# Kernel optimization log

Hardware: AMD Instinct MI355X
Metric: run time of the kernel (lower is better)

Reference implementation:

```python
import jax, jax.numpy as jnp
import numpy as np

IN, OUT, RANK = 512, 1024, 8
STEPS = 8  # fixed-step RK4 integration of the geodesic ODE over t in [0, 1]


def setup_inputs() -> dict:
    key = jax.random.key(0)
    ks = jax.random.split(key, 8)
    scale = 0.05
    x = jax.random.normal(ks[0], (8, 4096, IN), jnp.float32)
    # orthogonal init of U_0 [OUT, IN] (orthonormal columns, tall matrix)
    U0 = jnp.linalg.qr(jax.random.normal(ks[1], (OUT, IN), jnp.float32))[0]
    Wa = scale * jax.random.normal(ks[2], (IN, RANK), jnp.float32)
    La = scale * jax.random.normal(ks[3], (IN, RANK), jnp.float32)
    Ra = scale * jax.random.normal(ks[4], (IN, RANK), jnp.float32)
    Wb = scale * jax.random.normal(ks[5], (IN, RANK), jnp.float32)
    Lb = scale * jax.random.normal(ks[6], (OUT - IN, RANK), jnp.float32)
    Rb = scale * jax.random.normal(ks[7], (IN, RANK), jnp.float32)
    return {"x": x, "U0": U0, "Wa": Wa, "La": La, "Ra": Ra,
            "Wb": Wb, "Lb": Lb, "Rb": Rb}


def _geodesic_solve(U0, A, G):
    # Integrate dU/dt = U @ A + G, U(0) = U0, with RK4 over unit time.
    dt = 1.0 / STEPS
    f = lambda U: U @ A + G
    def step(U, _):
        k1 = f(U)
        k2 = f(U + 0.5 * dt * k1)
        k3 = f(U + 0.5 * dt * k2)
        k4 = f(U + dt * k3)
        return U + (dt / 6.0) * (k1 + 2.0 * k2 + 2.0 * k3 + k4), None
    U, _ = jax.lax.scan(step, U0, None, length=STEPS)
    return U


def reference(x, U0, Wa, La, Ra, Wb, Lb, Rb):
    # z: pooled context [B, IN]
    z = x.mean(axis=1)
    # low-rank controller -> skew-symmetric Lie-algebra drift A [IN, IN]
    a = z @ Wa                                      # [B, R]
    A = jnp.einsum('br,ir,jr->bij', a, La, Ra)      # [B, IN, IN]
    A_avg = (A - jnp.swapaxes(A, 1, 2)).mean(axis=0)  # skew, batch-averaged
    # low-rank forcing B [B, OUT-IN, IN], batch-averaged
    b = z @ Wb                                      # [B, R]
    B_avg = jnp.einsum('br,or,jr->boj', b, Lb, Rb).mean(axis=0)
    # pad top with zeros -> G [OUT, IN]
    G = jnp.concatenate([jnp.zeros((IN, IN), x.dtype), B_avg], axis=0)
    # geodesic/Lie ODE solve for the dynamic weight W [OUT, IN]
    W = _geodesic_solve(U0, A_avg, G)
    # final dense projection
    return x @ W.T
```

## Files before the change

kernel.cpp:

```cpp
#include <hip/hip_runtime.h>
#include <hip/hip_bf16.h>
#include <type_traits>
#include <cstdint>

#define IN_DIM   512
#define OUT_DIM  1024
#define RANKP    8
#define MROWS    32768

typedef float f32x4 __attribute__((ext_vector_type(4)));
typedef short s8vec __attribute__((ext_vector_type(8)));
typedef __bf16 b8vec __attribute__((ext_vector_type(8)));

template <typename V, typename = void>
struct mfma_ok : std::false_type {};
template <typename V>
struct mfma_ok<V, std::void_t<decltype(__builtin_amdgcn_mfma_f32_16x16x32_bf16(
    std::declval<V>(), std::declval<V>(), std::declval<f32x4>(), 0, 0, 0))>>
    : std::true_type {};
using frag_t = std::conditional_t<mfma_ok<s8vec>::value, s8vec, b8vec>;

__device__ __forceinline__ void async_copy16(void* lds, const void* g) {
    __builtin_amdgcn_global_load_lds(
        (const __attribute__((address_space(1))) void*)(uintptr_t)g,
        (__attribute__((address_space(3))) void*)(uint32_t)(uintptr_t)lds,
        16, 0, 0);
}

__device__ __forceinline__ unsigned short f2bf(float f) {
    unsigned int u = __float_as_uint(f);
    unsigned int r = (u + 0x7fffu + ((u >> 16) & 1u)) >> 16;
    return (unsigned short)r;
}

__global__ void __launch_bounds__(256) geo_k1(const float* __restrict__ x,
                                              unsigned short* __restrict__ xh,
                                              const float* __restrict__ Wa,
                                              const float* __restrict__ Wb,
                                              float* __restrict__ gsum) {
    const int tid  = threadIdx.x;
    const int c4   = (tid & 127) * 4;
    const int half = tid >> 7;
    const int r0   = blockIdx.x * 32 + half * 16;
    float4 s = {0.f, 0.f, 0.f, 0.f};
    for (int i = 0; i < 16; ++i) {
        const size_t base = (size_t)(r0 + i) * IN_DIM + c4;
        float4 v = *(const float4*)(x + base);
        s.x += v.x; s.y += v.y; s.z += v.z; s.w += v.w;
        ushort4 h;
        h.x = f2bf(v.x); h.y = f2bf(v.y); h.z = f2bf(v.z); h.w = f2bf(v.w);
        *(ushort4*)(xh + base) = h;
    }
    const float* wa = Wa + (size_t)c4 * 8;
    const float* wb = Wb + (size_t)c4 * 8;
    float av[8], bv[8];
#pragma unroll
    for (int r = 0; r < 8; ++r) {
        av[r] = s.x * wa[r] + s.y * wa[8 + r] + s.z * wa[16 + r] + s.w * wa[24 + r];
        bv[r] = s.x * wb[r] + s.y * wb[8 + r] + s.z * wb[16 + r] + s.w * wb[24 + r];
    }
#pragma unroll
    for (int off = 32; off; off >>= 1) {
#pragma unroll
        for (int r = 0; r < 8; ++r) {
            av[r] += __shfl_xor(av[r], off, 64);
            bv[r] += __shfl_xor(bv[r], off, 64);
        }
    }
    __shared__ float wred[4][16];
    const int lane = tid & 63, wave = tid >> 6;
    if (lane == 0) {
#pragma unroll
        for (int r = 0; r < 8; ++r) { wred[wave][r] = av[r]; wred[wave][8 + r] = bv[r]; }
    }
    __syncthreads();
    if (tid < 16) {
        float t = wred[0][tid] + wred[1][tid] + wred[2][tid] + wred[3][tid];
        atomicAdd(&gsum[tid], t);
    }
}

__global__ void geo_k2a(const float* __restrict__ gsum, const float* __restrict__ La,
                        const float* __restrict__ Ra, const float* __restrict__ Lb,
                        float* __restrict__ Vws, float* __restrict__ Lbp) {
    const int tid = threadIdx.x;
    const int i = blockIdx.x * 32 + (tid >> 3);
    const int r = tid & 7;
    const float sc = 1.0f / 32768.0f;
    const float ar = gsum[r] * sc;
    const float br = gsum[8 + r] * sc;
    Vws[i * 16 + r]     = ar * La[i * 8 + r];
    Vws[i * 16 + 8 + r] = Ra[i * 8 + r];
    Lbp[i * 8 + r]      = br * Lb[i * 8 + r];
}

__global__ void geo_k2b(const float* __restrict__ Vws, const float* __restrict__ Rb,
                        float* __restrict__ Gg, float* __restrict__ Zg) {
    __shared__ float sX[16][24];
    const int tid = threadIdx.x;
    const int i0 = blockIdx.x * 16;
    for (int e = tid; e < 384; e += 256) {
        const int row = e / 24, col = e - row * 24;
        sX[row][col] = (col < 16) ? Vws[(i0 + row) * 16 + col]
                                  : Rb[(i0 + row) * 8 + col - 16];
    }
    __syncthreads();
    {
        const int u = tid >> 4, v = tid & 15;
        float s = 0.f;
#pragma unroll
        for (int k = 0; k < 16; ++k) s += sX[k][u] * sX[k][v];
        atomicAdd(&Gg[tid], s);
    }
    if (tid < 128) {
        const int r = tid >> 4, u = tid & 15;
        float s = 0.f;
#pragma unroll
        for (int k = 0; k < 16; ++k) s += sX[k][16 + r] * sX[k][u];
        atomicAdd(&Zg[tid], s);
    }
}

__device__ __forceinline__ void mm16(float (*D)[16], float (*A)[16], float (*B)[16]) {
    const int tid = threadIdx.x;
    const int i = tid >> 4, j = tid & 15;
    float s = 0.f;
#pragma unroll
    for (int k = 0; k < 16; ++k) s += A[i][k] * B[k][j];
    __syncthreads();
    D[i][j] = s;
    __syncthreads();
}

__global__ void geo_k2c(const float* __restrict__ Gg, const float* __restrict__ Zg,
                        const float* __restrict__ Vws, const float* __restrict__ Rb,
                        float* __restrict__ VPws, float* __restrict__ RRws) {
    __shared__ float G16[16][16], Jm[16][16];
    __shared__ float C2m[16][16], C3m[16][16], C4m[16][16];
    __shared__ float Cp[16][16], Cq[16][16];
    __shared__ float Pi[16][16], Xi[16][16], T1[16][16], T2[16][16], Ct[16][16];
    __shared__ float Zm[8][16], Em[8][16];
    const int tid = threadIdx.x;
    const int i = tid >> 4, j = tid & 15;

    G16[i][j] = Gg[tid];
    float jm = 0.f;
    if (i < 8 && j == i + 8) jm = 1.f;
    if (i >= 8 && j == i - 8) jm = -1.f;
    Jm[i][j] = jm;
    if (tid < 128) Zm[tid >> 4][tid & 15] = Zg[tid];
    __syncthreads();

    mm16(T1, Jm, G16);  mm16(C2m, T1, Jm);
    mm16(T1, C2m, G16); mm16(C3m, T1, Jm);
    mm16(T1, C3m, G16); mm16(C4m, T1, Jm);

    const float h  = 0.125f;
    const float c1 = h, c2 = h * h * 0.5f, c3 = h * h * h * (1.f / 6.f),
                c4 = h * h * h * h * (1.f / 24.f);
    Cp[i][j] = c1 * Jm[i][j] + c2 * C2m[i][j] + c3 * C3m[i][j] + c4 * C4m[i][j];
    Cq[i][j] = c2 * Jm[i][j] + c3 * C2m[i][j] + c4 * C3m[i][j];
    Xi[i][j] = 0.f;
    __syncthreads();
    Pi[i][j] = Cp[i][j];
    __syncthreads();

    for (int it = 0; it < 7; ++it) {
        mm16(T1, Pi, G16);
        mm16(T2, T1, Cp);
        const float pij = Pi[i][j];
        Xi[i][j] += pij;
        Pi[i][j] = pij + Cp[i][j] + T2[i][j];
        __syncthreads();
    }

    mm16(T1, Cq, G16);
    mm16(T2, T1, Xi);
    Ct[i][j] = 8.f * Cq[i][j] + h * Xi[i][j] + T2[i][j];
    __syncthreads();

    if (tid < 128) {
        const int r = tid >> 4, u = tid & 15;
        float s = 0.f;
#pragma unroll
        for (int t = 0; t < 16; ++t) s += Zm[r][t] * Ct[t][u];
        Em[r][u] = s;
    }
    __syncthreads();

#pragma unroll
    for (int rr = 0; rr < 2; ++rr) {
        const int row = tid * 2 + rr;
        const float* vr = Vws + row * 16;
        float v[16];
#pragma unroll
        for (int q = 0; q < 4; ++q) {
            float4 t4 = *(const float4*)(vr + q * 4);
            v[q * 4] = t4.x; v[q * 4 + 1] = t4.y; v[q * 4 + 2] = t4.z; v[q * 4 + 3] = t4.w;
        }
#pragma unroll
        for (int u = 0; u < 16; ++u) {
            float s = 0.f;
#pragma unroll
            for (int k = 0; k < 16; ++k) s += v[k] * Pi[k][u];
            VPws[row * 16 + u] = s;
        }
#pragma unroll
        for (int r = 0; r < 8; ++r) {
            float s = Rb[row * 8 + r];
#pragma unroll
            for (int u = 0; u < 16; ++u) s += Em[r][u] * v[u];
            RRws[r * IN_DIM + row] = s;
        }
    }
}

__global__ void __launch_bounds__(256) geo_k34(const float* __restrict__ U0,
                                               const float* __restrict__ Vws,
                                               const float* __restrict__ VPws,
                                               const float* __restrict__ Lbp,
                                               const float* __restrict__ RRws,
                                               unsigned short* __restrict__ wh) {
    const int o   = blockIdx.x;
    const int tid = threadIdx.x;
    const int j0  = tid * 2;
    const float2 u0 = *(const float2*)(U0 + (size_t)o * IN_DIM + j0);

    const float* vpa = VPws + j0 * 16;
    const float* vpb = vpa + 16;
    float p[16];
#pragma unroll
    for (int u = 0; u < 16; ++u) p[u] = u0.x * vpa[u] + u0.y * vpb[u];
#pragma unroll
    for (int off = 32; off; off >>= 1) {
#pragma unroll
        for (int u = 0; u < 16; ++u) p[u] += __shfl_xor(p[u], off, 64);
    }
    __shared__ float wred[4][16];
    __shared__ float sY[16];
    const int lane = tid & 63, wave = tid >> 6;
    if (lane == 0) {
#pragma unroll
        for (int u = 0; u < 16; ++u) wred[wave][u] = p[u];
    }
    __syncthreads();
    if (tid < 16) sY[tid] = wred[0][tid] + wred[1][tid] + wred[2][tid] + wred[3][tid];
    __syncthreads();

    const float* va = Vws + j0 * 16;
    const float* vb = va + 16;
    float w0 = u0.x, w1 = u0.y;
#pragma unroll
    for (int u = 0; u < 16; ++u) {
        const float s = sY[u];
        w0 += s * va[u];
        w1 += s * vb[u];
    }
    if (o >= IN_DIM) {
        const int op = o - IN_DIM;
#pragma unroll
        for (int r = 0; r < 8; ++r) {
            const float lb = Lbp[op * 8 + r];
            w0 += lb * RRws[r * IN_DIM + j0];
            w1 += lb * RRws[r * IN_DIM + j0 + 1];
        }
    }
    ushort2 hv;
    hv.x = f2bf(w0); hv.y = f2bf(w1);
    *(ushort2*)(wh + (size_t)o * IN_DIM + j0) = hv;
}

__global__ void __launch_bounds__(256) geo_k5_gemm(const __hip_bfloat16* __restrict__ A,
                                                   const __hip_bfloat16* __restrict__ B,
                                                   float* __restrict__ C) {
    __shared__ __hip_bfloat16 As[128 * 32];
    __shared__ __hip_bfloat16 Bs[128 * 32];
    const int tid  = threadIdx.x;
    const int m0   = blockIdx.x * 128;
    const int n0   = blockIdx.y * 128;
    const int lane = tid & 63;
    const int wave = tid >> 6;
    const int wm   = (wave >> 1) * 64;
    const int wn   = (wave & 1) * 64;

    const int srow = tid >> 2;
    const int scol = (tid & 3) * 8;
    const __hip_bfloat16* gA0 = A + (size_t)(m0 + srow) * IN_DIM + scol;
    const __hip_bfloat16* gA1 = A + (size_t)(m0 + 64 + srow) * IN_DIM + scol;
    const __hip_bfloat16* gB0 = B + (size_t)(n0 + srow) * IN_DIM + scol;
    const __hip_bfloat16* gB1 = B + (size_t)(n0 + 64 + srow) * IN_DIM + scol;
    __hip_bfloat16* lA0 = As + (size_t)tid * 8;
    __hip_bfloat16* lA1 = As + (size_t)(tid + 256) * 8;
    __hip_bfloat16* lB0 = Bs + (size_t)tid * 8;
    __hip_bfloat16* lB1 = Bs + (size_t)(tid + 256) * 8;

    f32x4 acc[4][4];
#pragma unroll
    for (int t = 0; t < 4; ++t)
#pragma unroll
        for (int s = 0; s < 4; ++s) acc[t][s] = (f32x4){0.f, 0.f, 0.f, 0.f};

    const int aoff = (wm + (lane & 15)) * 32 + (lane >> 4) * 8;
    const int boff = (wn + (lane & 15)) * 32 + (lane >> 4) * 8;

    for (int kt = 0; kt < 16; ++kt) {
        const int k0 = kt * 32;
        __syncthreads();
        async_copy16(lA0, gA0 + k0);
        async_copy16(lA1, gA1 + k0);
        async_copy16(lB0, gB0 + k0);
        async_copy16(lB1, gB1 + k0);
        __syncthreads();

        frag_t af[4], bfr[4];
#pragma unroll
        for (int t = 0; t < 4; ++t) af[t] = *(const frag_t*)(As + aoff + t * 16 * 32);
#pragma unroll
        for (int s = 0; s < 4; ++s) bfr[s] = *(const frag_t*)(Bs + boff + s * 16 * 32);
#pragma unroll
        for (int t = 0; t < 4; ++t)
#pragma unroll
            for (int s = 0; s < 4; ++s)
                acc[t][s] = __builtin_amdgcn_mfma_f32_16x16x32_bf16(af[t], bfr[s], acc[t][s], 0, 0, 0);
    }

    const int cm = m0 + wm + (lane >> 4) * 4;
    const int cn = n0 + wn + (lane & 15);
#pragma unroll
    for (int t = 0; t < 4; ++t)
#pragma unroll
        for (int s = 0; s < 4; ++s)
#pragma unroll
            for (int v = 0; v < 4; ++v)
                C[(size_t)(cm + t * 16 + v) * OUT_DIM + cn + s * 16] = acc[t][s][v];
}

extern "C" void kernel_launch(void* const* d_in, const int* in_sizes, int n_in,
                              void* d_out, int out_size, void* d_ws, size_t ws_size,
                              hipStream_t stream) {
    const float* x  = (const float*)d_in[0];
    const float* U0 = (const float*)d_in[1];
    const float* Wa = (const float*)d_in[2];
    const float* La = (const float*)d_in[3];
    const float* Ra = (const float*)d_in[4];
    const float* Wb = (const float*)d_in[5];
    const float* Lb = (const float*)d_in[6];
    const float* Rb = (const float*)d_in[7];
    float* out = (float*)d_out;

    char* ws = (char*)d_ws;
    unsigned short* xh  = (unsigned short*)(ws);
    unsigned short* wh  = (unsigned short*)(ws + 33554432);
    float* acc  = (float*)(ws + 34603008);
    float* gsum = acc;
    float* Gg   = acc + 16;
    float* Zg   = acc + 272;
    float* Vws  = (float*)(ws + 34605056);
    float* Lbp  = (float*)(ws + 34637824);
    float* RRws = (float*)(ws + 34654208);
    float* VPws = (float*)(ws + 34670592);

    hipMemsetAsync(acc, 0, 2048, stream);
    geo_k1<<<1024, 256, 0, stream>>>(x, xh, Wa, Wb, gsum);
    geo_k2a<<<16, 256, 0, stream>>>(gsum, La, Ra, Lb, Vws, Lbp);
    geo_k2b<<<32, 256, 0, stream>>>(Vws, Rb, Gg, Zg);
    geo_k2c<<<1, 256, 0, stream>>>(Gg, Zg, Vws, Rb, VPws, RRws);
    geo_k34<<<1024, 256, 0, stream>>>(U0, Vws, VPws, Lbp, RRws, wh);
    geo_k5_gemm<<<dim3(256, 8), 256, 0, stream>>>((const __hip_bfloat16*)xh,
                                                  (const __hip_bfloat16*)wh, out);
}
```

Baseline: 312.0 us.

## Fuse small setup kernels into one block and widen GEMM K-tile with LDS swizzle

Replaces the memset plus atomic reductions and three small kernels (k2a, k2b, k2c) with per-block partial sums from k1 and a single one-block kernel that reduces them, builds V, computes the Gram matrices and the closed-form propagators. The goal is to cut launch overhead and atomic traffic. The GEMM separately doubles its K tile to 64 with an XOR-swizzled LDS layout, halving the number of barrier/load rounds and avoiding bank conflicts. The single-block kernel now does a serial 512-long Gram reduction, which adds some latency on one CU.

```diff
diff --git a/kernel.cpp b/kernel.cpp
--- a/kernel.cpp
+++ b/kernel.cpp
@@ -5,7 +5,6 @@
 
 #define IN_DIM   512
 #define OUT_DIM  1024
-#define RANKP    8
 #define MROWS    32768
 
 typedef float f32x4 __attribute__((ext_vector_type(4)));
@@ -37,7 +36,7 @@
                                               unsigned short* __restrict__ xh,
                                               const float* __restrict__ Wa,
                                               const float* __restrict__ Wb,
-                                              float* __restrict__ gsum) {
+                                              float* __restrict__ part) {
     const int tid  = threadIdx.x;
     const int c4   = (tid & 127) * 4;
     const int half = tid >> 7;
@@ -74,51 +73,9 @@
         for (int r = 0; r < 8; ++r) { wred[wave][r] = av[r]; wred[wave][8 + r] = bv[r]; }
     }
     __syncthreads();
-    if (tid < 16) {
-        float t = wred[0][tid] + wred[1][tid] + wred[2][tid] + wred[3][tid];
-        atomicAdd(&gsum[tid], t);
-    }
-}
-
-__global__ void geo_k2a(const float* __restrict__ gsum, const float* __restrict__ La,
-                        const float* __restrict__ Ra, const float* __restrict__ Lb,
-                        float* __restrict__ Vws, float* __restrict__ Lbp) {
-    const int tid = threadIdx.x;
-    const int i = blockIdx.x * 32 + (tid >> 3);
-    const int r = tid & 7;
-    const float sc = 1.0f / 32768.0f;
-    const float ar = gsum[r] * sc;
-    const float br = gsum[8 + r] * sc;
-    Vws[i * 16 + r]     = ar * La[i * 8 + r];
-    Vws[i * 16 + 8 + r] = Ra[i * 8 + r];
-    Lbp[i * 8 + r]      = br * Lb[i * 8 + r];
-}
-
-__global__ void geo_k2b(const float* __restrict__ Vws, const float* __restrict__ Rb,
-                        float* __restrict__ Gg, float* __restrict__ Zg) {
-    __shared__ float sX[16][24];
-    const int tid = threadIdx.x;
-    const int i0 = blockIdx.x * 16;
-    for (int e = tid; e < 384; e += 256) {
-        const int row = e / 24, col = e - row * 24;
-        sX[row][col] = (col < 16) ? Vws[(i0 + row) * 16 + col]
-                                  : Rb[(i0 + row) * 8 + col - 16];
-    }
-    __syncthreads();
-    {
-        const int u = tid >> 4, v = tid & 15;
-        float s = 0.f;
-#pragma unroll
-        for (int k = 0; k < 16; ++k) s += sX[k][u] * sX[k][v];
-        atomicAdd(&Gg[tid], s);
-    }
-    if (tid < 128) {
-        const int r = tid >> 4, u = tid & 15;
-        float s = 0.f;
-#pragma unroll
-        for (int k = 0; k < 16; ++k) s += sX[k][16 + r] * sX[k][u];
-        atomicAdd(&Zg[tid], s);
-    }
+    if (tid < 16)
+        part[(size_t)blockIdx.x * 16 + tid] =
+            wred[0][tid] + wred[1][tid] + wred[2][tid] + wred[3][tid];
 }
 
 __device__ __forceinline__ void mm16(float (*D)[16], float (*A)[16], float (*B)[16]) {
@@ -132,9 +89,19 @@
     __syncthreads();
 }
 
-__global__ void geo_k2c(const float* __restrict__ Gg, const float* __restrict__ Zg,
-                        const float* __restrict__ Vws, const float* __restrict__ Rb,
-                        float* __restrict__ VPws, float* __restrict__ RRws) {
+__global__ void __launch_bounds__(256) geo_k2(const float* __restrict__ part,
+                                              const float* __restrict__ La,
+                                              const float* __restrict__ Ra,
+                                              const float* __restrict__ Lb,
+                                              const float* __restrict__ Rb,
+                                              float* __restrict__ Vws,
+                                              float* __restrict__ Lbp,
+                                              float* __restrict__ VPws,
+                                              float* __restrict__ RRws) {
+    __shared__ float sV[IN_DIM][16];
+    __shared__ float sRb[IN_DIM][8];
+    __shared__ float red2[16][16];
+    __shared__ float gs[16];
     __shared__ float G16[16][16], Jm[16][16];
     __shared__ float C2m[16][16], C3m[16][16], C4m[16][16];
     __shared__ float Cp[16][16], Cq[16][16];
@@ -143,12 +110,52 @@
     const int tid = threadIdx.x;
     const int i = tid >> 4, j = tid & 15;
 
-    G16[i][j] = Gg[tid];
-    float jm = 0.f;
-    if (i < 8 && j == i + 8) jm = 1.f;
-    if (i >= 8 && j == i - 8) jm = -1.f;
-    Jm[i][j] = jm;
-    if (tid < 128) Zm[tid >> 4][tid & 15] = Zg[tid];
+    {
+        const int u = tid & 15, c = tid >> 4;
+        float s = 0.f;
+        for (int q = 0; q < 64; ++q) s += part[(size_t)(c * 64 + q) * 16 + u];
+        red2[c][u] = s;
+    }
+    __syncthreads();
+    if (tid < 16) {
+        float s = 0.f;
+#pragma unroll
+        for (int c = 0; c < 16; ++c) s += red2[c][tid];
+        gs[tid] = s * (1.0f / 32768.0f);
+    }
+    __syncthreads();
+
+    for (int rr = 0; rr < 2; ++rr) {
+        const int row = tid * 2 + rr;
+#pragma unroll
+        for (int r = 0; r < 8; ++r) {
+            const float vl = gs[r] * La[row * 8 + r];
+            const float vr = Ra[row * 8 + r];
+            sV[row][r]     = vl;
+            sV[row][8 + r] = vr;
+            Vws[row * 16 + r]     = vl;
+            Vws[row * 16 + 8 + r] = vr;
+            sRb[row][r] = Rb[row * 8 + r];
+            Lbp[row * 8 + r] = gs[8 + r] * Lb[row * 8 + r];
+        }
+    }
+    __syncthreads();
+
+    {
+        float s = 0.f;
+        for (int k = 0; k < IN_DIM; ++k) s += sV[k][i] * sV[k][j];
+        G16[i][j] = s;
+        float jm = 0.f;
+        if (i < 8 && j == i + 8) jm = 1.f;
+        if (i >= 8 && j == i - 8) jm = -1.f;
+        Jm[i][j] = jm;
+    }
+    if (tid < 128) {
+        const int r = tid >> 4, u = tid & 15;
+        float s = 0.f;
+        for (int k = 0; k < IN_DIM; ++k) s += sRb[k][r] * sV[k][u];
+        Zm[r][u] = s;
+    }
     __syncthreads();
 
     mm16(T1, Jm, G16);  mm16(C2m, T1, Jm);
@@ -191,13 +198,9 @@
 #pragma unroll
     for (int rr = 0; rr < 2; ++rr) {
         const int row = tid * 2 + rr;
-        const float* vr = Vws + row * 16;
         float v[16];
 #pragma unroll
-        for (int q = 0; q < 4; ++q) {
-            float4 t4 = *(const float4*)(vr + q * 4);
-            v[q * 4] = t4.x; v[q * 4 + 1] = t4.y; v[q * 4 + 2] = t4.z; v[q * 4 + 3] = t4.w;
-        }
+        for (int k = 0; k < 16; ++k) v[k] = sV[row][k];
 #pragma unroll
         for (int u = 0; u < 16; ++u) {
             float s = 0.f;
@@ -207,7 +210,7 @@
         }
 #pragma unroll
         for (int r = 0; r < 8; ++r) {
-            float s = Rb[row * 8 + r];
+            float s = sRb[row][r];
 #pragma unroll
             for (int u = 0; u < 16; ++u) s += Em[r][u] * v[u];
             RRws[r * IN_DIM + row] = s;
@@ -273,8 +276,8 @@
 __global__ void __launch_bounds__(256) geo_k5_gemm(const __hip_bfloat16* __restrict__ A,
                                                    const __hip_bfloat16* __restrict__ B,
                                                    float* __restrict__ C) {
-    __shared__ __hip_bfloat16 As[128 * 32];
-    __shared__ __hip_bfloat16 Bs[128 * 32];
+    __shared__ __hip_bfloat16 As[128 * 64];
+    __shared__ __hip_bfloat16 Bs[128 * 64];
     const int tid  = threadIdx.x;
     const int m0   = blockIdx.x * 128;
     const int n0   = blockIdx.y * 128;
@@ -283,16 +286,21 @@
     const int wm   = (wave >> 1) * 64;
     const int wn   = (wave & 1) * 64;
 
-    const int srow = tid >> 2;
-    const int scol = (tid & 3) * 8;
-    const __hip_bfloat16* gA0 = A + (size_t)(m0 + srow) * IN_DIM + scol;
-    const __hip_bfloat16* gA1 = A + (size_t)(m0 + 64 + srow) * IN_DIM + scol;
-    const __hip_bfloat16* gB0 = B + (size_t)(n0 + srow) * IN_DIM + scol;
-    const __hip_bfloat16* gB1 = B + (size_t)(n0 + 64 + srow) * IN_DIM + scol;
-    __hip_bfloat16* lA0 = As + (size_t)tid * 8;
-    __hip_bfloat16* lA1 = As + (size_t)(tid + 256) * 8;
-    __hip_bfloat16* lB0 = Bs + (size_t)tid * 8;
-    __hip_bfloat16* lB1 = Bs + (size_t)(tid + 256) * 8;
+    const int rowoff = lane >> 3;
+    const int gcol   = ((lane & 7) ^ rowoff) * 8;
+    const __hip_bfloat16* gA[4];
+    const __hip_bfloat16* gB[4];
+    char* lA[4];
+    char* lB[4];
+#pragma unroll
+    for (int j2 = 0; j2 < 4; ++j2) {
+        const int ri  = wave * 4 + j2;
+        const int row = ri * 8 + rowoff;
+        gA[j2] = A + (size_t)(m0 + row) * IN_DIM + gcol;
+        gB[j2] = B + (size_t)(n0 + row) * IN_DIM + gcol;
+        lA[j2] = (char*)As + ri * 1024 + lane * 16;
+        lB[j2] = (char*)Bs + ri * 1024 + lane * 16;
+    }
 
     f32x4 acc[4][4];
 #pragma unroll
@@ -300,28 +308,37 @@
 #pragma unroll
         for (int s = 0; s < 4; ++s) acc[t][s] = (f32x4){0.f, 0.f, 0.f, 0.f};
 
-    const int aoff = (wm + (lane & 15)) * 32 + (lane >> 4) * 8;
-    const int boff = (wn + (lane & 15)) * 32 + (lane >> 4) * 8;
-
-    for (int kt = 0; kt < 16; ++kt) {
-        const int k0 = kt * 32;
+    const int frow = lane & 15;
+    const int fsw  = lane & 7;
+    const int fk   = lane >> 4;
+
+    for (int kt = 0; kt < 8; ++kt) {
+        const int k0 = kt * 64;
         __syncthreads();
-        async_copy16(lA0, gA0 + k0);
-        async_copy16(lA1, gA1 + k0);
-        async_copy16(lB0, gB0 + k0);
-        async_copy16(lB1, gB1 + k0);
+#pragma unroll
+        for (int j2 = 0; j2 < 4; ++j2) {
+            async_copy16(lA[j2], gA[j2] + k0);
+            async_copy16(lB[j2], gB[j2] + k0);
+        }
         __syncthreads();
 
-        frag_t af[4], bfr[4];
-#pragma unroll
-        for (int t = 0; t < 4; ++t) af[t] = *(const frag_t*)(As + aoff + t * 16 * 32);
-#pragma unroll
-        for (int s = 0; s < 4; ++s) bfr[s] = *(const frag_t*)(Bs + boff + s * 16 * 32);
-#pragma unroll
-        for (int t = 0; t < 4; ++t)
+#pragma unroll
+        for (int h = 0; h < 2; ++h) {
+            frag_t af[4], bfr[4];
+#pragma unroll
+            for (int t = 0; t < 4; ++t)
+                af[t] = *(const frag_t*)((const char*)As +
+                        (size_t)(wm + t * 16 + frow) * 128 + (((h * 4 + fk) ^ fsw) * 16));
 #pragma unroll
             for (int s = 0; s < 4; ++s)
-                acc[t][s] = __builtin_amdgcn_mfma_f32_16x16x32_bf16(af[t], bfr[s], acc[t][s], 0, 0, 0);
+                bfr[s] = *(const frag_t*)((const char*)Bs +
+                        (size_t)(wn + s * 16 + frow) * 128 + (((h * 4 + fk) ^ fsw) * 16));
+#pragma unroll
+            for (int t = 0; t < 4; ++t)
+#pragma unroll
+                for (int s = 0; s < 4; ++s)
+                    acc[t][s] = __builtin_amdgcn_mfma_f32_16x16x32_bf16(af[t], bfr[s], acc[t][s], 0, 0, 0);
+        }
     }
 
     const int cm = m0 + wm + (lane >> 4) * 4;
@@ -351,20 +368,14 @@
     char* ws = (char*)d_ws;
     unsigned short* xh  = (unsigned short*)(ws);
     unsigned short* wh  = (unsigned short*)(ws + 33554432);
-    float* acc  = (float*)(ws + 34603008);
-    float* gsum = acc;
-    float* Gg   = acc + 16;
-    float* Zg   = acc + 272;
-    float* Vws  = (float*)(ws + 34605056);
-    float* Lbp  = (float*)(ws + 34637824);
-    float* RRws = (float*)(ws + 34654208);
-    float* VPws = (float*)(ws + 34670592);
-
-    hipMemsetAsync(acc, 0, 2048, stream);
-    geo_k1<<<1024, 256, 0, stream>>>(x, xh, Wa, Wb, gsum);
-    geo_k2a<<<16, 256, 0, stream>>>(gsum, La, Ra, Lb, Vws, Lbp);
-    geo_k2b<<<32, 256, 0, stream>>>(Vws, Rb, Gg, Zg);
-    geo_k2c<<<1, 256, 0, stream>>>(Gg, Zg, Vws, Rb, VPws, RRws);
+    float* part = (float*)(ws + 34603008);
+    float* Vws  = (float*)(ws + 34668544);
+    float* Lbp  = (float*)(ws + 34701312);
+    float* RRws = (float*)(ws + 34717696);
+    float* VPws = (float*)(ws + 34734080);
+
+    geo_k1<<<1024, 256, 0, stream>>>(x, xh, Wa, Wb, part);
+    geo_k2<<<1, 256, 0, stream>>>(part, La, Ra, Lb, Rb, Vws, Lbp, VPws, RRws);
     geo_k34<<<1024, 256, 0, stream>>>(U0, Vws, VPws, Lbp, RRws, wh);
     geo_k5_gemm<<<dim3(256, 8), 256, 0, stream>>>((const __hip_bfloat16*)xh,
                                                   (const __hip_bfloat16*)wh, out);
```

New measurement: 277.8 us. -11.0%, faster.
